# Kernel tuning notes

Hardware: AMD Instinct MI355X
Metric: run time of the kernel (lower is better)

## Reference

```python
import jax, jax.numpy as jnp
import numpy as np

IN_FEATURES = 4096
OUT_FEATURES = 11008
BLOCK_SIZE = 64
BITS = 4
RANGE_MAX = 2 ** (BITS - 1) - 1  # 7


def setup_inputs() -> dict:
    key = jax.random.key(0)
    k1, k2, k3, k4 = jax.random.split(key, 4)
    n_blocks = OUT_FEATURES * IN_FEATURES // BLOCK_SIZE
    x = jax.random.normal(k1, (4, 2048, IN_FEATURES), dtype=jnp.float32)
    # int4 codes in [-7, 7]; stored signed int. Use randint in [-7, 8).
    weight_quant = jax.random.randint(k2, (n_blocks, BLOCK_SIZE), -RANGE_MAX, RANGE_MAX + 1, dtype=jnp.int32)
    weight_absmax = jax.random.uniform(k3, (n_blocks, 1), dtype=jnp.float32, minval=1e-5, maxval=1.0)
    bias = jax.random.normal(k4, (OUT_FEATURES,), dtype=jnp.float32)
    return {"x": x, "weight_quant": weight_quant, "weight_absmax": weight_absmax, "bias": bias}


def reference(x, weight_quant, weight_absmax, bias):
    # Blockwise dequant: q/range_max * absmax per block, reshape to (out, in). padding=0.
    w = (weight_quant.astype(jnp.float32) / RANGE_MAX) * weight_absmax  # [n_blocks, block]
    w = w.reshape(OUT_FEATURES, IN_FEATURES)
    # F.linear: y = x @ W^T + b
    return jnp.einsum('bsi,oi->bso', x, w) + bias
```

## Files before the change

kernel.cpp:

```cpp
#include <hip/hip_runtime.h>


#define K_DIM 4096
#define N_DIM 11008
#define M_DIM 8192
#define NT_K 64
#define AB_OFF 98304
#define TILE_BYTES 2097152

typedef _Float16 f16;
typedef _Float16 f16x8 __attribute__((ext_vector_type(8)));
typedef float f32x16 __attribute__((ext_vector_type(16)));
typedef float fv4 __attribute__((ext_vector_type(4)));
typedef int iv4 __attribute__((ext_vector_type(4)));

__device__ __forceinline__ void gload16(const void* g, void* lds) {
  __builtin_amdgcn_global_load_lds(
      (__attribute__((address_space(1))) void*)g,
      (__attribute__((address_space(3))) void*)lds,
      16, 0, 0);
}

__global__ __launch_bounds__(256) void prep_kernel(const float* __restrict__ x,
                                                   f16* __restrict__ xo, int n16x,
                                                   const int* __restrict__ q,
                                                   const float* __restrict__ amax,
                                                   f16* __restrict__ wo, int n16w) {
  int i = blockIdx.x * blockDim.x + threadIdx.x;
  if (i < n16x) {
    const int lam = i & 63;
    const int F = (i >> 6) & 15;
    const int kk = (i >> 10) & 1;
    const int t = (i >> 11) & 63;
    const int mt = i >> 17;
    const int row = mt * 256 + ((F >> 1) << 5) + (lam & 31);
    const int kc = t * 64 + (kk << 5) + ((F & 1) << 4) + ((lam >> 5) << 3);
    const fv4* src = (const fv4*)(x + (size_t)row * K_DIM + kc);
    fv4 a = __builtin_nontemporal_load(src);
    fv4 b = __builtin_nontemporal_load(src + 1);
    f16x8 o;
    o[0] = (f16)a.x; o[1] = (f16)a.y; o[2] = (f16)a.z; o[3] = (f16)a.w;
    o[4] = (f16)b.x; o[5] = (f16)b.y; o[6] = (f16)b.z; o[7] = (f16)b.w;
    *(f16x8*)(xo + (size_t)i * 8) = o;
  } else {
    int j = i - n16x;
    if (j >= n16w) return;
    const int lam = j & 63;
    const int F = (j >> 6) & 15;
    const int kk = (j >> 10) & 1;
    const int t = (j >> 11) & 63;
    const int nt = j >> 17;
    const int row = nt * 256 + ((F >> 1) << 5) + (lam & 31);
    const int kc = t * 64 + (kk << 5) + ((F & 1) << 4) + ((lam >> 5) << 3);
    const size_t base = (size_t)row * K_DIM + kc;
    const iv4* src = (const iv4*)(q + base);
    iv4 a = __builtin_nontemporal_load(src);
    iv4 b = __builtin_nontemporal_load(src + 1);
    float s = amax[base >> 6] * (1.0f / 7.0f);
    f16x8 o;
    o[0] = (f16)((float)a.x * s); o[1] = (f16)((float)a.y * s);
    o[2] = (f16)((float)a.z * s); o[3] = (f16)((float)a.w * s);
    o[4] = (f16)((float)b.x * s); o[5] = (f16)((float)b.y * s);
    o[6] = (f16)((float)b.z * s); o[7] = (f16)((float)b.w * s);
    *(f16x8*)(wo + (size_t)j * 8) = o;
  }
}

__global__ __launch_bounds__(512, 2) void gemm_f16_bt(const f16* __restrict__ A,
                                                      const f16* __restrict__ B,
                                                      const float* __restrict__ bias,
                                                      float* __restrict__ C) {
  __shared__ __align__(16) char lds[163840];

  const int tid = threadIdx.x;
  const int w = tid >> 6;
  const int l = tid & 63;
  const int wr = w >> 2;
  const int wc = w & 3;

  const int wg = blockIdx.x;
  const int swz = (wg & 7) * 172 + (wg >> 3);
  const int mt = swz / 43;
  const int nt = swz % 43;
  const int m0 = mt * 256;
  const int n0 = nt * 256;

  const char* Abase = (const char*)A + (size_t)mt * TILE_BYTES + (w << 10) + (l << 4);
  const char* Bbase = (const char*)B + (size_t)nt * TILE_BYTES + (w << 10) + (l << 4);

  char* ldsc = (char*)lds;

#define STAGE_A(dst_off, koff)               \
  {                                          \
    char* d_ = ldsc + (dst_off) + (w << 10); \
    gload16(Abase + (koff), d_);             \
    gload16(Abase + (koff) + 8192, d_ + 8192); \
  }
#define STAGE_B(dst_off, koff)               \
  {                                          \
    char* d_ = ldsc + (dst_off) + (w << 10); \
    gload16(Bbase + (koff), d_);             \
    gload16(Bbase + (koff) + 8192, d_ + 8192); \
  }

  f32x16 acc[4][2];
#pragma unroll
  for (int i = 0; i < 4; ++i)
#pragma unroll
    for (int j = 0; j < 2; ++j) acc[i][j] = (f32x16)0.f;

  const int l16 = l << 4;
  const int aF0 = (wr << 3) << 10;
  const int bF0 = (wc << 2) << 10;

  STAGE_A(0, 0);
  STAGE_A(16384, 16384);
  STAGE_B(AB_OFF, 0);
  STAGE_B(AB_OFF + 16384, 16384);
  STAGE_A(32768, 32768);
  STAGE_A(32768 + 16384, 32768 + 16384);
  STAGE_B(AB_OFF + 32768, 32768);
  asm volatile("s_waitcnt vmcnt(6)" ::: "memory");
  __builtin_amdgcn_s_barrier();

  int ap = 0;
  int ap2 = 65536;

  for (int t = 0; t < NT_K; ++t) {
    const int p = t & 1;
    const int pn = p ^ 1;
    const int Bb = AB_OFF + p * 32768;
    const int Bn = AB_OFF + pn * 32768;
    const int t1 = (t + 1 < NT_K) ? (t + 1) : (NT_K - 1);
    const int t2 = (t + 2 < NT_K) ? (t + 2) : (NT_K - 1);
    const int k1 = t1 * 32768;
    const int k2 = t2 * 32768;

#pragma unroll
    for (int pi = 0; pi < 4; ++pi) {
      const int kk = pi >> 1;
      const int ks = pi & 1;

      f16x8 af[4], bf[2];
#pragma unroll
      for (int mf = 0; mf < 4; ++mf)
        af[mf] = *(const f16x8*)(ldsc + ap + kk * 16384 + aF0 + ((mf << 1) | ks) * 1024 + l16);
#pragma unroll
      for (int nf = 0; nf < 2; ++nf)
        bf[nf] = *(const f16x8*)(ldsc + Bb + kk * 16384 + bF0 + ((nf << 1) | ks) * 1024 + l16);

      if (pi == 0) {
        STAGE_B(Bn + 16384, k1 + 16384);
      } else if (pi == 1) {
        STAGE_A(ap2, k2);
      } else if (pi == 2) {
        STAGE_A(ap2 + 16384, k2 + 16384);
      } else {
        STAGE_B(Bb, k2);
      }

      __builtin_amdgcn_s_barrier();
      asm volatile("s_waitcnt lgkmcnt(0)" ::: "memory");
      __builtin_amdgcn_sched_barrier(0);
      __builtin_amdgcn_s_setprio(1);
#pragma unroll
      for (int mf = 0; mf < 4; ++mf)
#pragma unroll
        for (int nf = 0; nf < 2; ++nf)
          acc[mf][nf] = __builtin_amdgcn_mfma_f32_32x32x16_f16(af[mf], bf[nf], acc[mf][nf], 0, 0, 0);
      __builtin_amdgcn_s_setprio(0);
      if (pi == 3) asm volatile("s_waitcnt vmcnt(6)" ::: "memory");
      __builtin_amdgcn_s_barrier();
    }

    ap += 32768;  if (ap == AB_OFF) ap = 0;
    ap2 += 32768; if (ap2 == AB_OFF) ap2 = 0;
  }

  const int l31 = l & 31;
  const int rbase = 4 * (l >> 5);
  float bv[2];
#pragma unroll
  for (int nf = 0; nf < 2; ++nf) bv[nf] = bias[n0 + wc * 64 + nf * 32 + l31];
#pragma unroll
  for (int mf = 0; mf < 4; ++mf) {
#pragma unroll
    for (int nf = 0; nf < 2; ++nf) {
      const size_t col = n0 + wc * 64 + nf * 32 + l31;
#pragma unroll
      for (int qd = 0; qd < 4; ++qd) {
#pragma unroll
        for (int j = 0; j < 4; ++j) {
          const int row = m0 + wr * 128 + mf * 32 + rbase + 8 * qd + j;
          __builtin_nontemporal_store(acc[mf][nf][qd * 4 + j] + bv[nf],
                                      &C[(size_t)row * N_DIM + col]);
        }
      }
    }
  }
#undef STAGE_A
#undef STAGE_B
}

extern "C" void kernel_launch(void* const* d_in, const int* in_sizes, int n_in,
                              void* d_out, int out_size, void* d_ws, size_t ws_size,
                              hipStream_t stream) {
  const float* x = (const float*)d_in[0];
  const int* wq = (const int*)d_in[1];
  const float* amax = (const float*)d_in[2];
  const float* bias = (const float*)d_in[3];
  float* out = (float*)d_out;

  f16* Xh = (f16*)d_ws;
  f16* Wh = (f16*)((char*)d_ws + (size_t)M_DIM * K_DIM * 2);

  {
    int n16x = M_DIM * K_DIM / 8;
    int n16w = N_DIM * K_DIM / 8;
    int nthr = n16x + n16w;
    prep_kernel<<<(nthr + 255) / 256, 256, 0, stream>>>(x, Xh, n16x, wq, amax, Wh, n16w);
  }
  {
    dim3 grid((M_DIM / 256) * (N_DIM / 256));
    gemm_f16_bt<<<grid, 512, 0, stream>>>(Xh, Wh, bias, out);
  }
}
```

Before: 883.9 us.

## Double-buffer LDS fragments in registers and cut per-phase barriers in GEMM loop

Restructures the K-loop of the f16 MFMA GEMM so fragment reads from LDS for the next sub-step go into a second register set while MFMAs run on the current one. The first fragments of the next tile are prefetched before the loop advances. Barriers drop from two per sub-step to two per K-tile, removing most of the lgkmcnt stalls and barrier overhead. In exchange it uses more VGPRs. It also risks a race: a wave's STAGE_B into the current B buffer can now overwrite data other waves have not finished reading, because no barrier separates the last read from the overwrite.

```diff
diff --git a/kernel.cpp b/kernel.cpp
--- a/kernel.cpp
+++ b/kernel.cpp
@@ -66,6 +66,28 @@
   }
 }
 
+__device__ __forceinline__ void read_frags(const char* ldsc, int abase, int bbase, int kk, int ks,
+                                           int aF0, int bF0, int l16,
+                                           f16x8 (&af)[4], f16x8 (&bf)[2]) {
+#pragma unroll
+  for (int mf = 0; mf < 4; ++mf)
+    af[mf] = *(const f16x8*)(ldsc + abase + kk * 16384 + aF0 + (((mf << 1) | ks) << 10) + l16);
+#pragma unroll
+  for (int nf = 0; nf < 2; ++nf)
+    bf[nf] = *(const f16x8*)(ldsc + bbase + kk * 16384 + bF0 + (((nf << 1) | ks) << 10) + l16);
+}
+
+__device__ __forceinline__ void mfma8(const f16x8 (&af)[4], const f16x8 (&bf)[2],
+                                      f32x16 (&acc)[4][2]) {
+  __builtin_amdgcn_s_setprio(1);
+#pragma unroll
+  for (int mf = 0; mf < 4; ++mf)
+#pragma unroll
+    for (int nf = 0; nf < 2; ++nf)
+      acc[mf][nf] = __builtin_amdgcn_mfma_f32_32x32x16_f16(af[mf], bf[nf], acc[mf][nf], 0, 0, 0);
+  __builtin_amdgcn_s_setprio(0);
+}
+
 __global__ __launch_bounds__(512, 2) void gemm_f16_bt(const f16* __restrict__ A,
                                                       const f16* __restrict__ B,
                                                       const float* __restrict__ bias,
@@ -90,16 +112,16 @@
 
   char* ldsc = (char*)lds;
 
-#define STAGE_A(dst_off, koff)               \
-  {                                          \
-    char* d_ = ldsc + (dst_off) + (w << 10); \
-    gload16(Abase + (koff), d_);             \
+#define STAGE_A(dst_off, koff)                 \
+  {                                            \
+    char* d_ = ldsc + (dst_off) + (w << 10);   \
+    gload16(Abase + (koff), d_);               \
     gload16(Abase + (koff) + 8192, d_ + 8192); \
   }
-#define STAGE_B(dst_off, koff)               \
-  {                                          \
-    char* d_ = ldsc + (dst_off) + (w << 10); \
-    gload16(Bbase + (koff), d_);             \
+#define STAGE_B(dst_off, koff)                 \
+  {                                            \
+    char* d_ = ldsc + (dst_off) + (w << 10);   \
+    gload16(Bbase + (koff), d_);               \
     gload16(Bbase + (koff) + 8192, d_ + 8192); \
   }
 
@@ -110,8 +132,8 @@
     for (int j = 0; j < 2; ++j) acc[i][j] = (f32x16)0.f;
 
   const int l16 = l << 4;
-  const int aF0 = (wr << 3) << 10;
-  const int bF0 = (wc << 2) << 10;
+  const int aF0 = wr << 13;
+  const int bF0 = wc << 12;
 
   STAGE_A(0, 0);
   STAGE_A(16384, 16384);
@@ -126,6 +148,11 @@
   int ap = 0;
   int ap2 = 65536;
 
+  f16x8 afe[4], bfe[2];
+  f16x8 afo[4], bfo[2];
+
+  read_frags(ldsc, 0, AB_OFF, 0, 0, aF0, bF0, l16, afe, bfe);
+
   for (int t = 0; t < NT_K; ++t) {
     const int p = t & 1;
     const int pn = p ^ 1;
@@ -136,45 +163,28 @@
     const int k1 = t1 * 32768;
     const int k2 = t2 * 32768;
 
-#pragma unroll
-    for (int pi = 0; pi < 4; ++pi) {
-      const int kk = pi >> 1;
-      const int ks = pi & 1;
-
-      f16x8 af[4], bf[2];
-#pragma unroll
-      for (int mf = 0; mf < 4; ++mf)
-        af[mf] = *(const f16x8*)(ldsc + ap + kk * 16384 + aF0 + ((mf << 1) | ks) * 1024 + l16);
-#pragma unroll
-      for (int nf = 0; nf < 2; ++nf)
-        bf[nf] = *(const f16x8*)(ldsc + Bb + kk * 16384 + bF0 + ((nf << 1) | ks) * 1024 + l16);
-
-      if (pi == 0) {
-        STAGE_B(Bn + 16384, k1 + 16384);
-      } else if (pi == 1) {
-        STAGE_A(ap2, k2);
-      } else if (pi == 2) {
-        STAGE_A(ap2 + 16384, k2 + 16384);
-      } else {
-        STAGE_B(Bb, k2);
-      }
-
-      __builtin_amdgcn_s_barrier();
-      asm volatile("s_waitcnt lgkmcnt(0)" ::: "memory");
-      __builtin_amdgcn_sched_barrier(0);
-      __builtin_amdgcn_s_setprio(1);
-#pragma unroll
-      for (int mf = 0; mf < 4; ++mf)
-#pragma unroll
-        for (int nf = 0; nf < 2; ++nf)
-          acc[mf][nf] = __builtin_amdgcn_mfma_f32_32x32x16_f16(af[mf], bf[nf], acc[mf][nf], 0, 0, 0);
-      __builtin_amdgcn_s_setprio(0);
-      if (pi == 3) asm volatile("s_waitcnt vmcnt(6)" ::: "memory");
-      __builtin_amdgcn_s_barrier();
-    }
-
-    ap += 32768;  if (ap == AB_OFF) ap = 0;
-    ap2 += 32768; if (ap2 == AB_OFF) ap2 = 0;
+    read_frags(ldsc, ap, Bb, 0, 1, aF0, bF0, l16, afo, bfo);
+    STAGE_B(Bn + 16384, k1 + 16384);
+    mfma8(afe, bfe, acc);
+
+    read_frags(ldsc, ap, Bb, 1, 0, aF0, bF0, l16, afe, bfe);
+    STAGE_A(ap2, k2);
+    mfma8(afo, bfo, acc);
+    __builtin_amdgcn_s_barrier();
+
+    read_frags(ldsc, ap, Bb, 1, 1, aF0, bF0, l16, afo, bfo);
+    STAGE_A(ap2 + 16384, k2 + 16384);
+    mfma8(afe, bfe, acc);
+
+    STAGE_B(Bb, k2);
+    mfma8(afo, bfo, acc);
+    asm volatile("s_waitcnt vmcnt(6)" ::: "memory");
+    __builtin_amdgcn_s_barrier();
+
+    const int apN = (ap + 32768 == AB_OFF) ? 0 : ap + 32768;
+    read_frags(ldsc, apN, Bn, 0, 0, aF0, bF0, l16, afe, bfe);
+    ap = apN;
+    ap2 = (ap2 + 32768 == AB_OFF) ? 0 : ap2 + 32768;
   }
 
   const int l31 = l & 31;
```

Result: no change. 874.8 us (-1.0%).

## Load A fragments directly from global into registers, stage only B via LDS

Applied to the files above, without the earlier changes.

The A operand is now read straight from global memory into register double-buffers (aX/aY) instead of going through LDS. Only B is still staged in LDS, triple-buffered, which shrinks shared memory from 160KB to 96KB. The K-step schedule is restructured into two slabs per tile that interleave register loads of A, asynchronous B staging and MFMA work, with one barrier per tile. The aim is to cut LDS traffic and barriers. The cost is that each A row stripe is fetched four times (once per column wave) from L2, register pressure rises, and the compute now depends on global-load latency.

```diff
diff --git a/kernel.cpp b/kernel.cpp
--- a/kernel.cpp
+++ b/kernel.cpp
@@ -5,7 +5,6 @@
 #define N_DIM 11008
 #define M_DIM 8192
 #define NT_K 64
-#define AB_OFF 98304
 #define TILE_BYTES 2097152
 
 typedef _Float16 f16;
@@ -70,7 +69,7 @@
                                                       const f16* __restrict__ B,
                                                       const float* __restrict__ bias,
                                                       float* __restrict__ C) {
-  __shared__ __align__(16) char lds[163840];
+  __shared__ __align__(16) char lds[98304];
 
   const int tid = threadIdx.x;
   const int w = tid >> 6;
@@ -85,23 +84,38 @@
   const int m0 = mt * 256;
   const int n0 = nt * 256;
 
-  const char* Abase = (const char*)A + (size_t)mt * TILE_BYTES + (w << 10) + (l << 4);
-  const char* Bbase = (const char*)B + (size_t)nt * TILE_BYTES + (w << 10) + (l << 4);
-
+  const char* Astripe = (const char*)A + (size_t)mt * TILE_BYTES + (wr << 13) + (l << 4);
+  const char* Bstage = (const char*)B + (size_t)nt * TILE_BYTES + (w << 10) + (l << 4);
   char* ldsc = (char*)lds;
-
-#define STAGE_A(dst_off, koff)               \
-  {                                          \
-    char* d_ = ldsc + (dst_off) + (w << 10); \
-    gload16(Abase + (koff), d_);             \
-    gload16(Abase + (koff) + 8192, d_ + 8192); \
-  }
-#define STAGE_B(dst_off, koff)               \
-  {                                          \
-    char* d_ = ldsc + (dst_off) + (w << 10); \
-    gload16(Bbase + (koff), d_);             \
-    gload16(Bbase + (koff) + 8192, d_ + 8192); \
-  }
+  const int boff = (wc << 12) + (l << 4);
+
+#define LOAD_A(dst, tt, kk)                                            \
+  {                                                                    \
+    const char* s_ = Astripe + (size_t)(tt) * 32768 + ((kk) << 14);    \
+    _Pragma("unroll") for (int u = 0; u < 8; ++u)                      \
+        dst[u] = *(const f16x8*)(s_ + (u << 10));                      \
+  }
+#define STAGE_B2(slot, tt, h)                                 \
+  {                                                           \
+    const char* s_ = Bstage + (size_t)(tt) * 32768 + ((h) << 14); \
+    char* d_ = ldsc + (slot) + ((h) << 14) + (w << 10);       \
+    gload16(s_, d_);                                          \
+    gload16(s_ + 8192, d_ + 8192);                            \
+  }
+#define READ_B(dst, slot, kk)                                   \
+  {                                                             \
+    const char* p_ = ldsc + (slot) + ((kk) << 14) + boff;       \
+    _Pragma("unroll") for (int v = 0; v < 4; ++v)               \
+        dst[v] = *(const f16x8*)(p_ + (v << 10));               \
+  }
+#define MFMA_SLAB(a, b)                                                     \
+  __builtin_amdgcn_s_setprio(1);                                            \
+  _Pragma("unroll") for (int ks = 0; ks < 2; ++ks)                          \
+      _Pragma("unroll") for (int mf = 0; mf < 4; ++mf)                      \
+          _Pragma("unroll") for (int nf = 0; nf < 2; ++nf)                  \
+              acc[mf][nf] = __builtin_amdgcn_mfma_f32_32x32x16_f16(         \
+                  a[mf * 2 + ks], b[nf * 2 + ks], acc[mf][nf], 0, 0, 0);    \
+  __builtin_amdgcn_s_setprio(0);
 
   f32x16 acc[4][2];
 #pragma unroll
@@ -109,72 +123,39 @@
 #pragma unroll
     for (int j = 0; j < 2; ++j) acc[i][j] = (f32x16)0.f;
 
-  const int l16 = l << 4;
-  const int aF0 = (wr << 3) << 10;
-  const int bF0 = (wc << 2) << 10;
-
-  STAGE_A(0, 0);
-  STAGE_A(16384, 16384);
-  STAGE_B(AB_OFF, 0);
-  STAGE_B(AB_OFF + 16384, 16384);
-  STAGE_A(32768, 32768);
-  STAGE_A(32768 + 16384, 32768 + 16384);
-  STAGE_B(AB_OFF + 32768, 32768);
-  asm volatile("s_waitcnt vmcnt(6)" ::: "memory");
+  f16x8 aX[8], aY[8];
+  f16x8 bf0[4], bf1[4];
+
+  STAGE_B2(0, 0, 0);
+  STAGE_B2(0, 0, 1);
+  STAGE_B2(32768, 1, 0);
+  STAGE_B2(32768, 1, 1);
+  LOAD_A(aX, 0, 0);
+  asm volatile("s_waitcnt vmcnt(0)" ::: "memory");
   __builtin_amdgcn_s_barrier();
 
-  int ap = 0;
-  int ap2 = 65536;
-
+  int bCur = 0;
+  int bStg = 65536;
   for (int t = 0; t < NT_K; ++t) {
-    const int p = t & 1;
-    const int pn = p ^ 1;
-    const int Bb = AB_OFF + p * 32768;
-    const int Bn = AB_OFF + pn * 32768;
-    const int t1 = (t + 1 < NT_K) ? (t + 1) : (NT_K - 1);
-    const int t2 = (t + 2 < NT_K) ? (t + 2) : (NT_K - 1);
-    const int k1 = t1 * 32768;
-    const int k2 = t2 * 32768;
-
-#pragma unroll
-    for (int pi = 0; pi < 4; ++pi) {
-      const int kk = pi >> 1;
-      const int ks = pi & 1;
-
-      f16x8 af[4], bf[2];
-#pragma unroll
-      for (int mf = 0; mf < 4; ++mf)
-        af[mf] = *(const f16x8*)(ldsc + ap + kk * 16384 + aF0 + ((mf << 1) | ks) * 1024 + l16);
-#pragma unroll
-      for (int nf = 0; nf < 2; ++nf)
-        bf[nf] = *(const f16x8*)(ldsc + Bb + kk * 16384 + bF0 + ((nf << 1) | ks) * 1024 + l16);
-
-      if (pi == 0) {
-        STAGE_B(Bn + 16384, k1 + 16384);
-      } else if (pi == 1) {
-        STAGE_A(ap2, k2);
-      } else if (pi == 2) {
-        STAGE_A(ap2 + 16384, k2 + 16384);
-      } else {
-        STAGE_B(Bb, k2);
-      }
-
-      __builtin_amdgcn_s_barrier();
-      asm volatile("s_waitcnt lgkmcnt(0)" ::: "memory");
-      __builtin_amdgcn_sched_barrier(0);
-      __builtin_amdgcn_s_setprio(1);
-#pragma unroll
-      for (int mf = 0; mf < 4; ++mf)
-#pragma unroll
-        for (int nf = 0; nf < 2; ++nf)
-          acc[mf][nf] = __builtin_amdgcn_mfma_f32_32x32x16_f16(af[mf], bf[nf], acc[mf][nf], 0, 0, 0);
-      __builtin_amdgcn_s_setprio(0);
-      if (pi == 3) asm volatile("s_waitcnt vmcnt(6)" ::: "memory");
-      __builtin_amdgcn_s_barrier();
-    }
-
-    ap += 32768;  if (ap == AB_OFF) ap = 0;
-    ap2 += 32768; if (ap2 == AB_OFF) ap2 = 0;
+    const int tA = (t + 1 < NT_K) ? (t + 1) : (NT_K - 1);
+    const int tS = (t + 2 < NT_K) ? (t + 2) : (NT_K - 1);
+    const int bNxt = (bCur == 65536) ? 0 : bCur + 32768;
+
+    LOAD_A(aY, t, 1);
+    STAGE_B2(bStg, tS, 0);
+    READ_B(bf0, bCur, 0);
+    MFMA_SLAB(aX, bf0);
+
+    LOAD_A(aX, tA, 0);
+    STAGE_B2(bStg, tS, 1);
+    READ_B(bf1, bCur, 1);
+    MFMA_SLAB(aY, bf1);
+
+    asm volatile("s_waitcnt vmcnt(12)" ::: "memory");
+    __builtin_amdgcn_s_barrier();
+
+    bCur = bNxt;
+    bStg = (bStg == 65536) ? 0 : bStg + 32768;
   }
 
   const int l31 = l & 31;
@@ -198,8 +179,10 @@
       }
     }
   }
-#undef STAGE_A
-#undef STAGE_B
+#undef LOAD_A
+#undef STAGE_B2
+#undef READ_B
+#undef MFMA_SLAB
 }
 
 extern "C" void kernel_launch(void* const* d_in, const int* in_sizes, int n_in,
```

New measurement: 1.009 ms. 1.14x slower.

## Switch GEMM to 256x128 tiles with 4 waves and triple-buffered K=32 stages

Applied to the files above, without the earlier changes.

Shrinks the workgroup tile from 256x256 with 8 waves to 256x128 with 4 waves, and uses a K step of 32 with a three-slot LDS ring instead of the mixed A/B double and triple buffering. The prep kernel's packed layout for X and W is changed to match the new per-stage fragment order. The loop now has one barrier pair per K step instead of four per 64-K step, and LDS use drops to 72KB, which may allow more resident workgroups. In exchange, each workgroup reuses less data across the smaller tile, so global and L2 traffic for A rises.

```diff
diff --git a/kernel.cpp b/kernel.cpp
--- a/kernel.cpp
+++ b/kernel.cpp
@@ -4,9 +4,11 @@
 #define K_DIM 4096
 #define N_DIM 11008
 #define M_DIM 8192
-#define NT_K 64
-#define AB_OFF 98304
-#define TILE_BYTES 2097152
+#define NT 128
+#define A_STRIPE 2097152
+#define B_STRIPE 1048576
+#define SLOT 24576
+#define B_OFF 16384
 
 typedef _Float16 f16;
 typedef _Float16 f16x8 __attribute__((ext_vector_type(8)));
@@ -30,11 +32,10 @@
   if (i < n16x) {
     const int lam = i & 63;
     const int F = (i >> 6) & 15;
-    const int kk = (i >> 10) & 1;
-    const int t = (i >> 11) & 63;
+    const int t = (i >> 10) & 127;
     const int mt = i >> 17;
     const int row = mt * 256 + ((F >> 1) << 5) + (lam & 31);
-    const int kc = t * 64 + (kk << 5) + ((F & 1) << 4) + ((lam >> 5) << 3);
+    const int kc = t * 32 + ((F & 1) << 4) + ((lam >> 5) << 3);
     const fv4* src = (const fv4*)(x + (size_t)row * K_DIM + kc);
     fv4 a = __builtin_nontemporal_load(src);
     fv4 b = __builtin_nontemporal_load(src + 1);
@@ -46,12 +47,11 @@
     int j = i - n16x;
     if (j >= n16w) return;
     const int lam = j & 63;
-    const int F = (j >> 6) & 15;
-    const int kk = (j >> 10) & 1;
-    const int t = (j >> 11) & 63;
-    const int nt = j >> 17;
-    const int row = nt * 256 + ((F >> 1) << 5) + (lam & 31);
-    const int kc = t * 64 + (kk << 5) + ((F & 1) << 4) + ((lam >> 5) << 3);
+    const int F = (j >> 6) & 7;
+    const int t = (j >> 9) & 127;
+    const int nt = j >> 16;
+    const int row = nt * 128 + ((F >> 1) << 5) + (lam & 31);
+    const int kc = t * 32 + ((F & 1) << 4) + ((lam >> 5) << 3);
     const size_t base = (size_t)row * K_DIM + kc;
     const iv4* src = (const iv4*)(q + base);
     iv4 a = __builtin_nontemporal_load(src);
@@ -66,41 +66,42 @@
   }
 }
 
-__global__ __launch_bounds__(512, 2) void gemm_f16_bt(const f16* __restrict__ A,
+__global__ __launch_bounds__(256, 2) void gemm_f16_bt(const f16* __restrict__ A,
                                                       const f16* __restrict__ B,
                                                       const float* __restrict__ bias,
                                                       float* __restrict__ C) {
-  __shared__ __align__(16) char lds[163840];
+  __shared__ __align__(16) char lds[73728];
 
   const int tid = threadIdx.x;
   const int w = tid >> 6;
   const int l = tid & 63;
-  const int wr = w >> 2;
-  const int wc = w & 3;
+  const int wr = w >> 1;
+  const int wc = w & 1;
 
   const int wg = blockIdx.x;
-  const int swz = (wg & 7) * 172 + (wg >> 3);
-  const int mt = swz / 43;
-  const int nt = swz % 43;
+  const int swz = (wg & 7) * 344 + (wg >> 3);
+  const int mt = swz / 86;
+  const int ntile = swz % 86;
   const int m0 = mt * 256;
-  const int n0 = nt * 256;
+  const int n0 = ntile * 128;
 
-  const char* Abase = (const char*)A + (size_t)mt * TILE_BYTES + (w << 10) + (l << 4);
-  const char* Bbase = (const char*)B + (size_t)nt * TILE_BYTES + (w << 10) + (l << 4);
-
+  const char* Aw = (const char*)A + (size_t)mt * A_STRIPE + (w << 10) + (l << 4);
+  const char* Bw = (const char*)B + (size_t)ntile * B_STRIPE + (w << 10) + (l << 4);
   char* ldsc = (char*)lds;
 
-#define STAGE_A(dst_off, koff)               \
-  {                                          \
-    char* d_ = ldsc + (dst_off) + (w << 10); \
-    gload16(Abase + (koff), d_);             \
-    gload16(Abase + (koff) + 8192, d_ + 8192); \
-  }
-#define STAGE_B(dst_off, koff)               \
-  {                                          \
-    char* d_ = ldsc + (dst_off) + (w << 10); \
-    gload16(Bbase + (koff), d_);             \
-    gload16(Bbase + (koff) + 8192, d_ + 8192); \
+  const int aoff = (wr << 13) + (l << 4);
+  const int boff = B_OFF + (wc << 12) + (l << 4);
+
+#define STAGE(slot, tt)                                            \
+  {                                                                \
+    const char* sa_ = Aw + (size_t)(tt) * 16384;                   \
+    char* da_ = ldsc + (slot) + (w << 10);                         \
+    _Pragma("unroll") for (int u = 0; u < 4; ++u)                  \
+        gload16(sa_ + (u << 12), da_ + (u << 12));                 \
+    const char* sb_ = Bw + (size_t)(tt) * 8192;                    \
+    char* db_ = ldsc + (slot) + B_OFF + (w << 10);                 \
+    _Pragma("unroll") for (int v = 0; v < 2; ++v)                  \
+        gload16(sb_ + (v << 12), db_ + (v << 12));                 \
   }
 
   f32x16 acc[4][2];
@@ -109,72 +110,43 @@
 #pragma unroll
     for (int j = 0; j < 2; ++j) acc[i][j] = (f32x16)0.f;
 
-  const int l16 = l << 4;
-  const int aF0 = (wr << 3) << 10;
-  const int bF0 = (wc << 2) << 10;
-
-  STAGE_A(0, 0);
-  STAGE_A(16384, 16384);
-  STAGE_B(AB_OFF, 0);
-  STAGE_B(AB_OFF + 16384, 16384);
-  STAGE_A(32768, 32768);
-  STAGE_A(32768 + 16384, 32768 + 16384);
-  STAGE_B(AB_OFF + 32768, 32768);
+  STAGE(0, 0);
+  STAGE(SLOT, 1);
   asm volatile("s_waitcnt vmcnt(6)" ::: "memory");
   __builtin_amdgcn_s_barrier();
 
-  int ap = 0;
-  int ap2 = 65536;
+  int s0 = 0, s1 = SLOT, s2 = 2 * SLOT;
 
-  for (int t = 0; t < NT_K; ++t) {
-    const int p = t & 1;
-    const int pn = p ^ 1;
-    const int Bb = AB_OFF + p * 32768;
-    const int Bn = AB_OFF + pn * 32768;
-    const int t1 = (t + 1 < NT_K) ? (t + 1) : (NT_K - 1);
-    const int t2 = (t + 2 < NT_K) ? (t + 2) : (NT_K - 1);
-    const int k1 = t1 * 32768;
-    const int k2 = t2 * 32768;
+  for (int t = 0; t < NT; ++t) {
+    const int tS = (t + 2 < NT) ? (t + 2) : (NT - 1);
 
+    f16x8 af[8], bf[4];
 #pragma unroll
-    for (int pi = 0; pi < 4; ++pi) {
-      const int kk = pi >> 1;
-      const int ks = pi & 1;
+    for (int u = 0; u < 8; ++u)
+      af[u] = *(const f16x8*)(ldsc + s0 + aoff + (u << 10));
+#pragma unroll
+    for (int v = 0; v < 4; ++v)
+      bf[v] = *(const f16x8*)(ldsc + s0 + boff + (v << 10));
 
-      f16x8 af[4], bf[2];
+    STAGE(s2, tS);
+
+    __builtin_amdgcn_s_barrier();
+    asm volatile("s_waitcnt lgkmcnt(0)" ::: "memory");
+    __builtin_amdgcn_sched_barrier(0);
+    __builtin_amdgcn_s_setprio(1);
 #pragma unroll
-      for (int mf = 0; mf < 4; ++mf)
-        af[mf] = *(const f16x8*)(ldsc + ap + kk * 16384 + aF0 + ((mf << 1) | ks) * 1024 + l16);
-#pragma unroll
-      for (int nf = 0; nf < 2; ++nf)
-        bf[nf] = *(const f16x8*)(ldsc + Bb + kk * 16384 + bF0 + ((nf << 1) | ks) * 1024 + l16);
-
-      if (pi == 0) {
-        STAGE_B(Bn + 16384, k1 + 16384);
-      } else if (pi == 1) {
-        STAGE_A(ap2, k2);
-      } else if (pi == 2) {
-        STAGE_A(ap2 + 16384, k2 + 16384);
-      } else {
-        STAGE_B(Bb, k2);
-      }
-
-      __builtin_amdgcn_s_barrier();
-      asm volatile("s_waitcnt lgkmcnt(0)" ::: "memory");
-      __builtin_amdgcn_sched_barrier(0);
-      __builtin_amdgcn_s_setprio(1);
+    for (int ks = 0; ks < 2; ++ks)
 #pragma unroll
       for (int mf = 0; mf < 4; ++mf)
 #pragma unroll
         for (int nf = 0; nf < 2; ++nf)
-          acc[mf][nf] = __builtin_amdgcn_mfma_f32_32x32x16_f16(af[mf], bf[nf], acc[mf][nf], 0, 0, 0);
-      __builtin_amdgcn_s_setprio(0);
-      if (pi == 3) asm volatile("s_waitcnt vmcnt(6)" ::: "memory");
-      __builtin_amdgcn_s_barrier();
-    }
+          acc[mf][nf] = __builtin_amdgcn_mfma_f32_32x32x16_f16(
+              af[mf * 2 + ks], bf[nf * 2 + ks], acc[mf][nf], 0, 0, 0);
+    __builtin_amdgcn_s_setprio(0);
+    asm volatile("s_waitcnt vmcnt(6)" ::: "memory");
+    __builtin_amdgcn_s_barrier();
 
-    ap += 32768;  if (ap == AB_OFF) ap = 0;
-    ap2 += 32768; if (ap2 == AB_OFF) ap2 = 0;
+    const int tmp = s0; s0 = s1; s1 = s2; s2 = tmp;
   }
 
   const int l31 = l & 31;
@@ -198,8 +170,7 @@
       }
     }
   }
-#undef STAGE_A
-#undef STAGE_B
+#undef STAGE
 }
 
 extern "C" void kernel_launch(void* const* d_in, const int* in_sizes, int n_in,
@@ -221,7 +192,7 @@
     prep_kernel<<<(nthr + 255) / 256, 256, 0, stream>>>(x, Xh, n16x, wq, amax, Wh, n16w);
   }
   {
-    dim3 grid((M_DIM / 256) * (N_DIM / 256));
-    gemm_f16_bt<<<grid, 512, 0, stream>>>(Xh, Wh, bias, out);
+    dim3 grid((M_DIM / 256) * (N_DIM / 128));
+    gemm_f16_bt<<<grid, 256, 0, stream>>>(Xh, Wh, bias, out);
   }
 }
```

New measurement: 884.6 us. Within noise of the previous version (+0.1%).
